# Optimization experiments

Hardware: AMD Instinct MI355X
Metric: run time of the kernel (lower is better)

The kernel has to match this reference:

```python
import jax, jax.numpy as jnp
import numpy as np

DIM = 256; CTX_DIM = 256; K = 7; SK = 5; NH = 4  # num_heads*2
HD = DIM // NH; SCALE = HD ** -0.5
H = 64; W = 64; HC = 56; WC = 56
LN_EPS = 1e-6; BN_EPS = 1e-5


def make_bias_idx(k, h, w):
    # Faithful port of ContMix.generate_idx + apply_rpb index construction.
    rs = 2 * k - 1
    idx_h = np.arange(k); idx_w = np.arange(k)
    idx_k = (idx_h[:, None] * rs + idx_w).reshape(-1)
    rep_h = np.ones(k, np.int64); rep_h[k // 2] = h - (k - 1)
    rep_w = np.ones(k, np.int64); rep_w[k // 2] = w - (k - 1)
    bias_hw = np.repeat(idx_h, rep_h)[:, None] * rs + np.repeat(idx_w, rep_w)  # (h, w)
    bias_idx = (bias_hw[..., None] + idx_k).reshape(-1, k * k)                 # (h*w, k^2)
    return jnp.asarray(bias_idx[::-1].copy())  # torch.flip along dim 0


def window_idx(n, k):
    # NATTEN-style clamped neighborhood window starts.
    s = np.clip(np.arange(n) - k // 2, 0, n - k)
    return jnp.asarray(s[:, None] + np.arange(k))  # (n, k)


BIDX1 = make_bias_idx(SK, H, W)
BIDX2 = make_bias_idx(K, H, W)
IDXI_S = window_idx(H, SK); IDXJ_S = window_idx(W, SK)
IDXI_L = window_idx(H, K);  IDXJ_L = window_idx(W, K)


def ln2d(x, g, b):
    # LayerNorm over channel dim per spatial location, x: (B, C, H, W)
    mu = x.mean(1, keepdims=True)
    var = ((x - mu) ** 2).mean(1, keepdims=True)
    return (x - mu) * jax.lax.rsqrt(var + LN_EPS) * g[None, :, None, None] + b[None, :, None, None]


def conv1x1(x, Wt):
    return jnp.einsum('oc,bchw->bohw', Wt, x)


def apply_rpb(attn, rpb, bias_idx, h, w):
    g = rpb.shape[0]
    r = rpb.reshape(g, -1)[:, bias_idx]  # (g, h*w, k^2)
    return attn + r.reshape(1, g, h, w, -1)


def na2d_av(attn, value, k, idx_i, idx_j):
    # attn: (B, G, H, W, k^2), value: (B, G, H, W, C)
    B, G, h, w, _ = attn.shape
    v = value[:, :, idx_i]        # (B, G, H, k, W, C)
    v = v[:, :, :, :, idx_j]      # (B, G, H, k, W, k, C)
    a = attn.reshape(B, G, h, w, k, k)
    return jnp.einsum('bghwpq,bghpwqc->bghwc', a, v)


def contmix_forward(x, ctx, Wq, gq, bq, Wk, gk, bk, Wproj, rpb1, rpb2, Wdy, bn_g, bn_b):
    B = x.shape[0]
    q = ln2d(conv1x1(x, Wq), gq, bq) * SCALE                       # (B, DIM, H, W)
    # AdaptiveAvgPool2d(7) on 56x56 -> exact 8x8 bins
    kctx = ctx.reshape(B, CTX_DIM, 7, HC // 7, 7, WC // 7).mean((3, 5))
    kf = ln2d(conv1x1(kctx, Wk), gk, bk)                            # (B, DIM, 7, 7)
    q = q.reshape(B, NH, HD, H * W)
    kf = kf.reshape(B, NH, HD, 49)
    wgt = jnp.einsum('bgcn,bgcl->bgnl', q, kf)                      # (B, 4, HW, 49)
    wgt = jnp.einsum('ml,bgnl->bgnm', Wproj, wgt)                   # (B, 4, HW, 74)
    wgt = wgt.reshape(B, NH, H, W, SK * SK + K * K)
    attn1 = wgt[:, :NH // 2, :, :, :SK * SK]                        # group1, 25
    attn2 = wgt[:, NH // 2:, :, :, SK * SK:]                        # group2, 49
    attn1 = jax.nn.softmax(apply_rpb(attn1, rpb1, BIDX1, H, W), -1)
    attn2 = jax.nn.softmax(apply_rpb(attn2, rpb2, BIDX2, H, W), -1)
    # 'b (m g c) h w -> m b g h w c', m=2, g=2
    v = x.reshape(B, 2, NH // 2, HD, H, W).transpose(1, 0, 2, 4, 5, 3)
    x1 = na2d_av(attn1, v[0], SK, IDXI_S, IDXJ_S)                   # (B, 2, H, W, HD)
    x2 = na2d_av(attn2, v[1], K, IDXI_L, IDXJ_L)
    out = jnp.concatenate([x1, x2], axis=1)                         # (B, 4, H, W, HD)
    out = out.transpose(0, 1, 4, 2, 3).reshape(B, DIM, H, W)
    out = conv1x1(out, Wdy)
    # BatchNorm2d in eval mode: running_mean=0, running_var=1
    out = out * (bn_g * jax.lax.rsqrt(jnp.float32(1.0) + BN_EPS))[None, :, None, None] + bn_b[None, :, None, None]
    return out


def setup_inputs() -> dict:
    key = jax.random.key(0)
    ks = jax.random.split(key, 10)
    d = {}
    d['x'] = jax.random.normal(ks[0], (4, DIM, H, W), jnp.float32)
    d['ctx'] = jax.random.normal(ks[1], (4, CTX_DIM, HC, WC), jnp.float32)
    d['Wq'] = jax.random.normal(ks[2], (DIM, DIM), jnp.float32) * 0.02
    d['gq'] = jnp.ones((DIM,), jnp.float32)
    d['bq'] = jnp.zeros((DIM,), jnp.float32)
    d['Wk'] = jax.random.normal(ks[3], (DIM, CTX_DIM), jnp.float32) * 0.02
    d['gk'] = jnp.ones((DIM,), jnp.float32)
    d['bk'] = jnp.zeros((DIM,), jnp.float32)
    d['Wproj'] = jax.random.normal(ks[4], (SK * SK + K * K, 49), jnp.float32) * 0.1
    d['rpb1'] = jax.random.normal(ks[5], (NH // 2, 2 * SK - 1, 2 * SK - 1), jnp.float32) * 0.02
    d['rpb2'] = jax.random.normal(ks[6], (NH // 2, 2 * K - 1, 2 * K - 1), jnp.float32) * 0.02
    d['Wdy'] = jax.random.normal(ks[7], (DIM, DIM), jnp.float32) * 0.02
    d['bn_g'] = jnp.ones((DIM,), jnp.float32)
    d['bn_b'] = jnp.zeros((DIM,), jnp.float32)
    return d


def reference(x, ctx, Wq, gq, bq, Wk, gk, bk, Wproj, rpb1, rpb2, Wdy, bn_g, bn_b):
    return contmix_forward(x, ctx, Wq, gq, bq, Wk, gk, bk, Wproj, rpb1, rpb2, Wdy, bn_g, bn_b)
```

## Files before the change

### kernel.cpp

```cpp
#include <hip/hip_runtime.h>

#define DEV __device__ __forceinline__

typedef __bf16 bf16x8 __attribute__((ext_vector_type(8)));
typedef __bf16 bf16x4 __attribute__((ext_vector_type(4)));
typedef float floatx4 __attribute__((ext_vector_type(4)));

__global__ __launch_bounds__(256)
void prep_kernel(const float* __restrict__ Wq, const float* __restrict__ Wdy,
                 const float* __restrict__ ctx, const float* __restrict__ x,
                 __bf16* __restrict__ wqb, __bf16* __restrict__ wdyb,
                 float* __restrict__ kctx, __bf16* __restrict__ xt) {
  __shared__ float tile[64][65];
  int bid = blockIdx.x, t = threadIdx.x;
  if (bid < 256) {
    int i = bid * 256 + t;
    wqb[i]  = (__bf16)Wq[i];
    wdyb[i] = (__bf16)Wdy[i];
  } else if (bid < 512) {
    int bc = (bid - 256) * 4 + (t >> 6);
    const float* src = ctx + (size_t)bc * (56 * 56);
    int w = t & 63;
#pragma unroll
    for (int pi = 0; pi < 7; ++pi) {
      float s = 0.f;
      if (w < 56) {
#pragma unroll
        for (int di = 0; di < 8; ++di) s += src[(pi * 8 + di) * 56 + w];
      }
      s += __shfl_down(s, 4);
      s += __shfl_down(s, 2);
      s += __shfl_down(s, 1);
      if (w < 56 && (w & 7) == 0)
        kctx[(size_t)bc * 49 + pi * 7 + (w >> 3)] = s * (1.f / 64.f);
    }
  } else {
    int idx = bid - 512;
    int b = idx >> 8, c0 = ((idx >> 6) & 3) * 64, n0 = (idx & 63) * 64;
    int lane = t & 63, rg = t >> 6;
    const float* src = x + ((size_t)b * 256 + c0) * 4096 + n0;
    for (int i = rg; i < 64; i += 4) tile[i][lane] = src[(size_t)i * 4096 + lane];
    __syncthreads();
    __bf16* dst = xt + ((size_t)b * 4096 + n0) * 256 + c0;
    for (int i = rg; i < 64; i += 4) dst[(size_t)i * 256 + lane] = (__bf16)tile[lane][i];
  }
}

__global__ __launch_bounds__(256)
void kf_ln_kernel(const float* __restrict__ kctx, const float* __restrict__ Wk,
                  const float* __restrict__ gk, const float* __restrict__ bk,
                  float* __restrict__ kf) {
  int b = blockIdx.x / 49, l = blockIdx.x % 49;
  __shared__ float xs[256];
  __shared__ float r1[4], r2[4];
  int o = threadIdx.x;
  xs[o] = kctx[((size_t)b * 256 + o) * 49 + l];
  __syncthreads();
  const float* wrow = Wk + (size_t)o * 256;
  float acc = 0.f;
#pragma unroll 8
  for (int c = 0; c < 256; c += 4) {
    float4 wv = *(const float4*)(wrow + c);
    acc += wv.x * xs[c] + wv.y * xs[c + 1] + wv.z * xs[c + 2] + wv.w * xs[c + 3];
  }
  float s1 = acc, s2 = acc * acc;
#pragma unroll
  for (int off = 32; off > 0; off >>= 1) {
    s1 += __shfl_down(s1, off);
    s2 += __shfl_down(s2, off);
  }
  int wv_ = o >> 6, ln = o & 63;
  if (ln == 0) { r1[wv_] = s1; r2[wv_] = s2; }
  __syncthreads();
  float mu  = (r1[0] + r1[1] + r1[2] + r1[3]) * (1.f / 256.f);
  float var = (r2[0] + r2[1] + r2[2] + r2[3]) * (1.f / 256.f) - mu * mu;
  float rstd = rsqrtf(var + 1e-6f);
  kf[((size_t)b * 256 + o) * 49 + l] = (acc - mu) * rstd * gk[o] + bk[o];
}

__global__ __launch_bounds__(256)
void kfp_kernel(const float* __restrict__ kf, const float* __restrict__ Wproj,
                __bf16* __restrict__ kfpT) {
  int bg = blockIdx.x; int b = bg >> 2, g = bg & 3;
  int m0 = blockIdx.y * 16;
  __shared__ float kfs[64][50];
  __shared__ float wps[16][50];
  int t = threadIdx.x;
  for (int i = t; i < 64 * 49; i += 256) {
    int d = i / 49, l = i % 49;
    kfs[d][l] = kf[((size_t)b * 256 + g * 64 + d) * 49 + l];
  }
  for (int i = t; i < 16 * 49; i += 256) {
    int m = i / 49, l = i % 49;
    wps[m][l] = (m0 + m < 74) ? Wproj[(m0 + m) * 49 + l] : 0.f;
  }
  __syncthreads();
  for (int i = t; i < 64 * 16; i += 256) {
    int d = i >> 4, m = i & 15;
    float s = 0.f;
    if (m0 + m < 74) {
#pragma unroll 7
      for (int l = 0; l < 49; ++l) s += kfs[d][l] * wps[m][l];
    }
    kfpT[(size_t)bg * 5120 + (m0 + m) * 64 + d] = (__bf16)s;
  }
}

DEV int rep_idx(int p, int kc, int t1, int sub) {
  return p < kc ? p : (p < t1 ? kc : p - sub);
}

template <int KK>
DEV void softmax_write(const float* wms, const float* rpb_s, __bf16* __restrict__ attnL,
                       int bg, int n_glob, int t) {
  constexpr int CNT = KK * KK;
  constexpr int RS  = 2 * KK - 1;
  constexpr int KC  = KK / 2;
  constexpr int T1  = KC + (64 - KK + 1);
  constexpr int SUB = 64 - KK;
  constexpr int MLO = (KK == 5) ? 0 : 25;
  constexpr int PW  = (KK == 5) ? 32 : 56;
  int h = n_glob >> 6, w = n_glob & 63;
  int rh = rep_idx(63 - h, KC, T1, SUB);
  int rw = rep_idx(63 - w, KC, T1, SUB);
  float vals[CNT];
  float mx = -1e30f;
#pragma unroll
  for (int m = 0; m < CNT; ++m) {
    int ki = m / KK, kj = m % KK;
    float v = wms[t * 81 + MLO + m] + rpb_s[(rh + ki) * RS + rw + kj];
    vals[m] = v; mx = fmaxf(mx, v);
  }
  float ssum = 0.f;
#pragma unroll
  for (int m = 0; m < CNT; ++m) { float e = __expf(vals[m] - mx); vals[m] = e; ssum += e; }
  float inv = 1.f / ssum;
  __bf16 hv[PW];
#pragma unroll
  for (int m = 0; m < PW; ++m) hv[m] = (__bf16)(m < CNT ? vals[m] * inv : 0.f);
  __bf16* ap = attnL + ((size_t)bg * 4096 + n_glob) * 56;
#pragma unroll
  for (int i = 0; i < PW / 8; ++i) *(bf16x8*)(ap + i * 8) = *(bf16x8*)&hv[i * 8];
}

__global__ __launch_bounds__(256, 1)
void qattn_kernel(const __bf16* __restrict__ Wb, const __bf16* __restrict__ XT,
                  const __bf16* __restrict__ kfpT,
                  const float* __restrict__ gq, const float* __restrict__ bq,
                  const float* __restrict__ rpb1, const float* __restrict__ rpb2,
                  __bf16* __restrict__ attnL) {
  __shared__ float wms[256 * 81];
  __shared__ float rpb_s[500];
  __shared__ float gqs[256], bqs[256];
  __shared__ float red_s[256], red_q[256];
  __shared__ float st_mu[64], st_rs[64];
  __bf16* As  = (__bf16*)wms;
  __bf16* Bs  = (__bf16*)wms + 8192;
  __bf16* Aat = (__bf16*)wms;

  int b  = blockIdx.z;
  int n0 = blockIdx.x * 64;
  int t  = threadIdx.x;
  int lane = t & 63, wv = t >> 6;
  int col = lane & 15, quad = lane >> 4;

  gqs[t] = gq[t] * 0.125f;
  bqs[t] = bq[t] * 0.125f;
  for (int i = t; i < 162; i += 256) rpb_s[i] = rpb1[i];
  for (int i = t; i < 338; i += 256) rpb_s[162 + i] = rpb2[i];

  floatx4 acc[4][4];
#pragma unroll
  for (int i = 0; i < 4; ++i)
#pragma unroll
    for (int j = 0; j < 4; ++j) acc[i][j] = {0.f, 0.f, 0.f, 0.f};

  int rowA = t >> 1, halfA = (t & 1) * 16;
  int rowB = t >> 2, kB = (t & 3) * 8;
  const __bf16* wp  = Wb + (size_t)rowA * 256 + halfA;
  const __bf16* wp2 = wp + 128 * 256;
  const __bf16* xp  = XT + ((size_t)b * 4096 + n0 + rowB) * 256 + kB;
  bf16x8 ra0a = *(const bf16x8*)wp;
  bf16x8 ra0b = *(const bf16x8*)(wp + 8);
  bf16x8 ra1a = *(const bf16x8*)wp2;
  bf16x8 ra1b = *(const bf16x8*)(wp2 + 8);
  bf16x8 rb   = *(const bf16x8*)xp;

  for (int c0 = 0; c0 < 256; c0 += 32) {
    *(bf16x8*)&As[rowA * 32 + halfA]             = ra0a;
    *(bf16x8*)&As[rowA * 32 + halfA + 8]         = ra0b;
    *(bf16x8*)&As[(128 + rowA) * 32 + halfA]     = ra1a;
    *(bf16x8*)&As[(128 + rowA) * 32 + halfA + 8] = ra1b;
    *(bf16x8*)&Bs[rowB * 32 + kB]                = rb;
    __syncthreads();
    if (c0 + 32 < 256) {
      ra0a = *(const bf16x8*)(wp  + c0 + 32);
      ra0b = *(const bf16x8*)(wp  + c0 + 40);
      ra1a = *(const bf16x8*)(wp2 + c0 + 32);
      ra1b = *(const bf16x8*)(wp2 + c0 + 40);
      rb   = *(const bf16x8*)(xp  + c0 + 32);
    }
    bf16x8 fa[4], fb[4];
#pragma unroll
    for (int i = 0; i < 4; ++i)
      fa[i] = *(const bf16x8*)&As[(wv * 64 + i * 16 + col) * 32 + quad * 8];
#pragma unroll
    for (int j = 0; j < 4; ++j)
      fb[j] = *(const bf16x8*)&Bs[(j * 16 + col) * 32 + quad * 8];
#pragma unroll
    for (int i = 0; i < 4; ++i)
#pragma unroll
      for (int j = 0; j < 4; ++j)
        acc[i][j] = __builtin_amdgcn_mfma_f32_16x16x32_bf16(fa[i], fb[j], acc[i][j], 0, 0, 0);
    __syncthreads();
  }

  float sj[4], qj[4];
#pragma unroll
  for (int j = 0; j < 4; ++j) {
    float s = 0.f, q = 0.f;
#pragma unroll
    for (int i = 0; i < 4; ++i)
#pragma unroll
      for (int r = 0; r < 4; ++r) { float v = acc[i][j][r]; s += v; q += v * v; }
    s += __shfl_xor(s, 16); s += __shfl_xor(s, 32);
    q += __shfl_xor(q, 16); q += __shfl_xor(q, 32);
    sj[j] = s; qj[j] = q;
  }
  if (quad == 0) {
#pragma unroll
    for (int j = 0; j < 4; ++j) {
      red_s[wv * 64 + j * 16 + col] = sj[j];
      red_q[wv * 64 + j * 16 + col] = qj[j];
    }
  }
  __syncthreads();
  if (t < 64) {
    float s = red_s[t] + red_s[64 + t] + red_s[128 + t] + red_s[192 + t];
    float q = red_q[t] + red_q[64 + t] + red_q[128 + t] + red_q[192 + t];
    float mu  = s * (1.f / 256.f);
    float var = q * (1.f / 256.f) - mu * mu;
    st_mu[t] = mu;
    st_rs[t] = rsqrtf(var + 1e-6f);
  }
  __syncthreads();

#pragma unroll
  for (int j = 0; j < 4; ++j) {
    float mu = st_mu[j * 16 + col], rs = st_rs[j * 16 + col];
#pragma unroll
    for (int i = 0; i < 4; ++i) {
      __bf16 pk[4];
#pragma unroll
      for (int r = 0; r < 4; ++r) {
        int o = wv * 64 + i * 16 + quad * 4 + r;
        pk[r] = (__bf16)((acc[i][j][r] - mu) * rs * gqs[o] + bqs[o]);
      }
      *(bf16x4*)&Aat[(wv * 64 + j * 16 + col) * 72 + i * 16 + quad * 4] = *(bf16x4*)pk;
    }
  }
  __syncthreads();

  bf16x8 fa2[2][4], fb2[2][5];
  const __bf16* kp = kfpT + (size_t)(b * 4 + wv) * 5120;
#pragma unroll
  for (int ks = 0; ks < 2; ++ks) {
#pragma unroll
    for (int a = 0; a < 4; ++a)
      fa2[ks][a] = *(const bf16x8*)&Aat[(wv * 64 + a * 16 + col) * 72 + ks * 32 + quad * 8];
#pragma unroll
    for (int nt = 0; nt < 5; ++nt)
      fb2[ks][nt] = *(const bf16x8*)&kp[(nt * 16 + col) * 64 + ks * 32 + quad * 8];
  }
  floatx4 acc2[4][5];
#pragma unroll
  for (int a = 0; a < 4; ++a)
#pragma unroll
    for (int nt = 0; nt < 5; ++nt) acc2[a][nt] = {0.f, 0.f, 0.f, 0.f};
#pragma unroll
  for (int ks = 0; ks < 2; ++ks)
#pragma unroll
    for (int a = 0; a < 4; ++a)
#pragma unroll
      for (int nt = 0; nt < 5; ++nt)
        acc2[a][nt] = __builtin_amdgcn_mfma_f32_16x16x32_bf16(fa2[ks][a], fb2[ks][nt], acc2[a][nt], 0, 0, 0);
  __syncthreads();

#pragma unroll
  for (int a = 0; a < 4; ++a)
#pragma unroll
    for (int nt = 0; nt < 5; ++nt)
#pragma unroll
      for (int r = 0; r < 4; ++r)
        wms[(wv * 64 + a * 16 + quad * 4 + r) * 81 + nt * 16 + col] = acc2[a][nt][r];
  __syncthreads();

  int g2 = t >> 6;
  int n_glob = n0 + (t & 63);
  int bg = b * 4 + g2;
  if (g2 < 2) softmax_write<5>(wms, rpb_s + g2 * 81,              attnL, bg, n_glob, t);
  else        softmax_write<7>(wms, rpb_s + 162 + (g2 - 2) * 169, attnL, bg, n_glob, t);
}

template <int MODE>
__global__ __launch_bounds__(256, 2)
void conv_mfma_kernel(const __bf16* __restrict__ Wb, const __bf16* __restrict__ Xin,
                      void* __restrict__ Yout, float* __restrict__ stats,
                      const float* __restrict__ bn_g, const float* __restrict__ bn_b) {
  int b  = blockIdx.z;
  int n0 = blockIdx.x * 128;
  int o0 = blockIdx.y * 128;
  __shared__ __bf16 As[128 * 32];
  __shared__ __bf16 Bs[128 * 32];
  int t = threadIdx.x;
  int lane = t & 63, wv = t >> 6;
  int mq = (wv & 1) * 64, nq = (wv >> 1) * 64;
  int col = lane & 15, quad = lane >> 4;
  floatx4 acc[4][4];
#pragma unroll
  for (int i = 0; i < 4; ++i)
#pragma unroll
    for (int j = 0; j < 4; ++j) acc[i][j] = {0.f, 0.f, 0.f, 0.f};
  int sm = t >> 1, sk = (t & 1) << 4;
  for (int c0 = 0; c0 < 256; c0 += 32) {
    const __bf16* wsrc = Wb + (size_t)(o0 + sm) * 256 + c0 + sk;
    *(bf16x8*)&As[sm * 32 + sk]     = *(const bf16x8*)wsrc;
    *(bf16x8*)&As[sm * 32 + sk + 8] = *(const bf16x8*)(wsrc + 8);
    const __bf16* xsrc;
    if (MODE == 0) {
      xsrc = Xin + ((size_t)b * 4096 + n0 + sm) * 256 + c0 + sk;
    } else {
      int c = c0 + sk, g = c >> 6, c64 = c & 63;
      xsrc = Xin + (((size_t)(b * 4 + g)) * 4096 + n0 + sm) * 64 + c64;
    }
    *(bf16x8*)&Bs[sm * 32 + sk]     = *(const bf16x8*)xsrc;
    *(bf16x8*)&Bs[sm * 32 + sk + 8] = *(const bf16x8*)(xsrc + 8);
    __syncthreads();
    bf16x8 fa[4], fb[4];
#pragma unroll
    for (int i = 0; i < 4; ++i)
      fa[i] = *(const bf16x8*)&As[(mq + i * 16 + col) * 32 + quad * 8];
#pragma unroll
    for (int j = 0; j < 4; ++j)
      fb[j] = *(const bf16x8*)&Bs[(nq + j * 16 + col) * 32 + quad * 8];
#pragma unroll
    for (int i = 0; i < 4; ++i)
#pragma unroll
      for (int j = 0; j < 4; ++j)
        acc[i][j] = __builtin_amdgcn_mfma_f32_16x16x32_bf16(fa[i], fb[j], acc[i][j], 0, 0, 0);
    __syncthreads();
  }
  {
    float* Yf = (float*)Yout + (size_t)b * 256 * 4096;
#pragma unroll
    for (int i = 0; i < 4; ++i) {
#pragma unroll
      for (int r = 0; r < 4; ++r) {
        int o = o0 + mq + i * 16 + quad * 4 + r;
        float scale = bn_g[o] * 0.9999950000374997f;
        float shift = bn_b[o];
        float* yrow = Yf + (size_t)o * 4096 + n0 + nq + col;
#pragma unroll
        for (int j = 0; j < 4; ++j) yrow[j * 16] = acc[i][j][r] * scale + shift;
      }
    }
  }
}

template <int KK>
DEV void na2d_body(const __bf16* __restrict__ attnL, const __bf16* __restrict__ XT,
                   __bf16* __restrict__ midT, __bf16* xs, int bg, int h0, int chalf, int t) {
  constexpr int CNT = KK * KK, KC = KK / 2, SMAX = 64 - KK;
  constexpr int ROWS = KK + 3;
  constexpr int PW = (KK == 5) ? 32 : 56;
  int b = bg >> 2, g = bg & 3;
  int si0 = min(max(h0 - KC, 0), SMAX);
  {
    int sn = t >> 2, sc = t & 3;
    const __bf16* src = XT + ((size_t)b * 4096 + sn) * 256 + g * 64 + chalf * 32 + sc * 8;
#pragma unroll
    for (int r = 0; r < ROWS; ++r) {
      int gr = min(si0 + r, 63);
      *(bf16x8*)&xs[(r * 64 + sn) * 40 + sc * 8] = *(const bf16x8*)(src + (size_t)gr * 64 * 256);
    }
  }
  __syncthreads();
  int w = t >> 2, cg = t & 3;
  int sj = min(max(w - KC, 0), SMAX);
#pragma unroll
  for (int h4 = 0; h4 < 4; ++h4) {
    int h = h0 + h4;
    int base = min(max(h - KC, 0), SMAX) - si0;
    bf16x8 avh[PW / 8];
    const __bf16* ap = attnL + ((size_t)bg * 4096 + h * 64 + w) * 56;
#pragma unroll
    for (int i = 0; i < PW / 8; ++i) avh[i] = *(const bf16x8*)(ap + i * 8);
    float av[CNT];
#pragma unroll
    for (int m = 0; m < CNT; ++m) av[m] = (float)avh[m / 8][m % 8];
    float acc[8] = {};
#pragma unroll
    for (int p = 0; p < KK; ++p) {
      const __bf16* xr = &xs[((base + p) * 64 + sj) * 40 + cg * 8];
#pragma unroll
      for (int q = 0; q < KK; ++q) {
        bf16x8 v = *(const bf16x8*)(xr + q * 40);
        float a = av[p * KK + q];
#pragma unroll
        for (int e = 0; e < 8; ++e) acc[e] += a * (float)v[e];
      }
    }
    __bf16 hv[8];
#pragma unroll
    for (int e = 0; e < 8; ++e) hv[e] = (__bf16)acc[e];
    *(bf16x8*)&midT[((size_t)bg * 4096 + h * 64 + w) * 64 + chalf * 32 + cg * 8] = *(bf16x8*)hv;
  }
}

__global__ __launch_bounds__(256)
void na2d_kernel(const __bf16* __restrict__ attnL, const __bf16* __restrict__ XT,
                 __bf16* __restrict__ midT) {
  __shared__ __bf16 xs[10 * 64 * 40];
  int bg = blockIdx.x, h0 = blockIdx.y * 4, chalf = blockIdx.z, t = threadIdx.x;
  if ((bg & 3) < 2) na2d_body<5>(attnL, XT, midT, xs, bg, h0, chalf, t);
  else              na2d_body<7>(attnL, XT, midT, xs, bg, h0, chalf, t);
}

extern "C" void kernel_launch(void* const* d_in, const int* in_sizes, int n_in,
                              void* d_out, int out_size, void* d_ws, size_t ws_size,
                              hipStream_t stream) {
  const float* x     = (const float*)d_in[0];
  const float* ctx   = (const float*)d_in[1];
  const float* Wq    = (const float*)d_in[2];
  const float* gq    = (const float*)d_in[3];
  const float* bq    = (const float*)d_in[4];
  const float* Wk    = (const float*)d_in[5];
  const float* gk    = (const float*)d_in[6];
  const float* bk    = (const float*)d_in[7];
  const float* Wproj = (const float*)d_in[8];
  const float* rpb1  = (const float*)d_in[9];
  const float* rpb2  = (const float*)d_in[10];
  const float* Wdy   = (const float*)d_in[11];
  const float* bn_g  = (const float*)d_in[12];
  const float* bn_b  = (const float*)d_in[13];
  float* out = (float*)d_out;

  float* ws     = (float*)d_ws;
  float* kctx   = ws;
  float* kf     = kctx + 50176;
  __bf16* attnL = (__bf16*)(kf + 50176);
  __bf16* wqb   = attnL + 3670016;
  __bf16* wdyb  = wqb + 65536;
  __bf16* kfpT  = wdyb + 65536;
  __bf16* XT    = kfpT + 81920;
  __bf16* midT  = XT + 4194304;

  prep_kernel<<<dim3(1536), dim3(256), 0, stream>>>(Wq, Wdy, ctx, x, wqb, wdyb, kctx, XT);
  kf_ln_kernel<<<dim3(196), dim3(256), 0, stream>>>(kctx, Wk, gk, bk, kf);
  kfp_kernel<<<dim3(16, 5), dim3(256), 0, stream>>>(kf, Wproj, kfpT);
  qattn_kernel<<<dim3(64, 1, 4), dim3(256), 0, stream>>>(wqb, XT, kfpT, gq, bq, rpb1, rpb2, attnL);
  na2d_kernel<<<dim3(16, 16, 2), dim3(256), 0, stream>>>(attnL, XT, midT);
  conv_mfma_kernel<1><<<dim3(32, 2, 4), dim3(256), 0, stream>>>(wdyb, midT, out, nullptr, bn_g, bn_b);
}
```

Before: 162.1 us.

## Halve qattn spatial tile for more blocks and add register prefetch to conv GEMM

The fused q-projection/attention kernel now handles 32 spatial positions per block instead of 64. That halves its shared-memory footprint and accumulator count, allows two blocks per CU, and doubles the grid to 512 blocks so the 256 CUs are better filled. The trade-off is that every block reloads the full weight matrix, and only half the threads do the softmax phase. Separately, the final conv GEMM now prefetches the next K-slice into registers before the shared-memory stores, overlapping global loads with MFMA work.

Measured after the change: 163.9 us. Within noise of the previous version (+1.1%).

```diff
diff --git a/kernel.cpp b/kernel.cpp
--- a/kernel.cpp
+++ b/kernel.cpp
@@ -112,7 +112,7 @@
 
 template <int KK>
 DEV void softmax_write(const float* wms, const float* rpb_s, __bf16* __restrict__ attnL,
-                       int bg, int n_glob, int t) {
+                       int bg, int n_glob, int row) {
   constexpr int CNT = KK * KK;
   constexpr int RS  = 2 * KK - 1;
   constexpr int KC  = KK / 2;
@@ -128,7 +128,7 @@
 #pragma unroll
   for (int m = 0; m < CNT; ++m) {
     int ki = m / KK, kj = m % KK;
-    float v = wms[t * 81 + MLO + m] + rpb_s[(rh + ki) * RS + rw + kj];
+    float v = wms[row * 81 + MLO + m] + rpb_s[(rh + ki) * RS + rw + kj];
     vals[m] = v; mx = fmaxf(mx, v);
   }
   float ssum = 0.f;
@@ -143,23 +143,23 @@
   for (int i = 0; i < PW / 8; ++i) *(bf16x8*)(ap + i * 8) = *(bf16x8*)&hv[i * 8];
 }
 
-__global__ __launch_bounds__(256, 1)
+__global__ __launch_bounds__(256, 2)
 void qattn_kernel(const __bf16* __restrict__ Wb, const __bf16* __restrict__ XT,
                   const __bf16* __restrict__ kfpT,
                   const float* __restrict__ gq, const float* __restrict__ bq,
                   const float* __restrict__ rpb1, const float* __restrict__ rpb2,
                   __bf16* __restrict__ attnL) {
-  __shared__ float wms[256 * 81];
+  __shared__ float wms[128 * 81];
   __shared__ float rpb_s[500];
   __shared__ float gqs[256], bqs[256];
-  __shared__ float red_s[256], red_q[256];
-  __shared__ float st_mu[64], st_rs[64];
+  __shared__ float red_s[128], red_q[128];
+  __shared__ float st_mu[32], st_rs[32];
   __bf16* As  = (__bf16*)wms;
   __bf16* Bs  = (__bf16*)wms + 8192;
   __bf16* Aat = (__bf16*)wms;
 
   int b  = blockIdx.z;
-  int n0 = blockIdx.x * 64;
+  int n0 = blockIdx.x * 32;
   int t  = threadIdx.x;
   int lane = t & 63, wv = t >> 6;
   int col = lane & 15, quad = lane >> 4;
@@ -169,55 +169,52 @@
   for (int i = t; i < 162; i += 256) rpb_s[i] = rpb1[i];
   for (int i = t; i < 338; i += 256) rpb_s[162 + i] = rpb2[i];
 
-  floatx4 acc[4][4];
+  floatx4 acc[4][2];
 #pragma unroll
   for (int i = 0; i < 4; ++i)
 #pragma unroll
-    for (int j = 0; j < 4; ++j) acc[i][j] = {0.f, 0.f, 0.f, 0.f};
-
-  int rowA = t >> 1, halfA = (t & 1) * 16;
-  int rowB = t >> 2, kB = (t & 3) * 8;
-  const __bf16* wp  = Wb + (size_t)rowA * 256 + halfA;
-  const __bf16* wp2 = wp + 128 * 256;
-  const __bf16* xp  = XT + ((size_t)b * 4096 + n0 + rowB) * 256 + kB;
-  bf16x8 ra0a = *(const bf16x8*)wp;
-  bf16x8 ra0b = *(const bf16x8*)(wp + 8);
-  bf16x8 ra1a = *(const bf16x8*)wp2;
-  bf16x8 ra1b = *(const bf16x8*)(wp2 + 8);
-  bf16x8 rb   = *(const bf16x8*)xp;
+    for (int j = 0; j < 2; ++j) acc[i][j] = {0.f, 0.f, 0.f, 0.f};
+
+  const __bf16* wp = Wb + (size_t)t * 256;
+  int rowB = t >> 3, kB = (t & 7) * 4;
+  const __bf16* xp = XT + ((size_t)b * 4096 + n0 + rowB) * 256 + kB;
+  bf16x8 ra0 = *(const bf16x8*)(wp + 0);
+  bf16x8 ra1 = *(const bf16x8*)(wp + 8);
+  bf16x8 ra2 = *(const bf16x8*)(wp + 16);
+  bf16x8 ra3 = *(const bf16x8*)(wp + 24);
+  bf16x4 rb  = *(const bf16x4*)xp;
 
   for (int c0 = 0; c0 < 256; c0 += 32) {
-    *(bf16x8*)&As[rowA * 32 + halfA]             = ra0a;
-    *(bf16x8*)&As[rowA * 32 + halfA + 8]         = ra0b;
-    *(bf16x8*)&As[(128 + rowA) * 32 + halfA]     = ra1a;
-    *(bf16x8*)&As[(128 + rowA) * 32 + halfA + 8] = ra1b;
-    *(bf16x8*)&Bs[rowB * 32 + kB]                = rb;
+    *(bf16x8*)&As[t * 32 + 0]  = ra0;
+    *(bf16x8*)&As[t * 32 + 8]  = ra1;
+    *(bf16x8*)&As[t * 32 + 16] = ra2;
+    *(bf16x8*)&As[t * 32 + 24] = ra3;
+    *(bf16x4*)&Bs[rowB * 32 + kB] = rb;
     __syncthreads();
     if (c0 + 32 < 256) {
-      ra0a = *(const bf16x8*)(wp  + c0 + 32);
-      ra0b = *(const bf16x8*)(wp  + c0 + 40);
-      ra1a = *(const bf16x8*)(wp2 + c0 + 32);
-      ra1b = *(const bf16x8*)(wp2 + c0 + 40);
-      rb   = *(const bf16x8*)(xp  + c0 + 32);
-    }
-    bf16x8 fa[4], fb[4];
+      ra0 = *(const bf16x8*)(wp + c0 + 32);
+      ra1 = *(const bf16x8*)(wp + c0 + 40);
+      ra2 = *(const bf16x8*)(wp + c0 + 48);
+      ra3 = *(const bf16x8*)(wp + c0 + 56);
+      rb  = *(const bf16x4*)(xp + c0 + 32);
+    }
+    bf16x8 fa[4], fb[2];
 #pragma unroll
     for (int i = 0; i < 4; ++i)
       fa[i] = *(const bf16x8*)&As[(wv * 64 + i * 16 + col) * 32 + quad * 8];
 #pragma unroll
-    for (int j = 0; j < 4; ++j)
+    for (int j = 0; j < 2; ++j)
       fb[j] = *(const bf16x8*)&Bs[(j * 16 + col) * 32 + quad * 8];
 #pragma unroll
     for (int i = 0; i < 4; ++i)
 #pragma unroll
-      for (int j = 0; j < 4; ++j)
+      for (int j = 0; j < 2; ++j)
         acc[i][j] = __builtin_amdgcn_mfma_f32_16x16x32_bf16(fa[i], fb[j], acc[i][j], 0, 0, 0);
     __syncthreads();
   }
 
-  float sj[4], qj[4];
-#pragma unroll
-  for (int j = 0; j < 4; ++j) {
+#pragma unroll
+  for (int j = 0; j < 2; ++j) {
     float s = 0.f, q = 0.f;
 #pragma unroll
     for (int i = 0; i < 4; ++i)
@@ -225,19 +222,15 @@
       for (int r = 0; r < 4; ++r) { float v = acc[i][j][r]; s += v; q += v * v; }
     s += __shfl_xor(s, 16); s += __shfl_xor(s, 32);
     q += __shfl_xor(q, 16); q += __shfl_xor(q, 32);
-    sj[j] = s; qj[j] = q;
-  }
-  if (quad == 0) {
-#pragma unroll
-    for (int j = 0; j < 4; ++j) {
-      red_s[wv * 64 + j * 16 + col] = sj[j];
-      red_q[wv * 64 + j * 16 + col] = qj[j];
-    }
-  }
-  __syncthreads();
-  if (t < 64) {
-    float s = red_s[t] + red_s[64 + t] + red_s[128 + t] + red_s[192 + t];
-    float q = red_q[t] + red_q[64 + t] + red_q[128 + t] + red_q[192 + t];
+    if (quad == 0) {
+      red_s[wv * 32 + j * 16 + col] = s;
+      red_q[wv * 32 + j * 16 + col] = q;
+    }
+  }
+  __syncthreads();
+  if (t < 32) {
+    float s = red_s[t] + red_s[32 + t] + red_s[64 + t] + red_s[96 + t];
+    float q = red_q[t] + red_q[32 + t] + red_q[64 + t] + red_q[96 + t];
     float mu  = s * (1.f / 256.f);
     float var = q * (1.f / 256.f) - mu * mu;
     st_mu[t] = mu;
@@ -246,7 +239,7 @@
   __syncthreads();
 
 #pragma unroll
-  for (int j = 0; j < 4; ++j) {
+  for (int j = 0; j < 2; ++j) {
     float mu = st_mu[j * 16 + col], rs = st_rs[j * 16 + col];
 #pragma unroll
     for (int i = 0; i < 4; ++i) {
@@ -256,50 +249,52 @@
         int o = wv * 64 + i * 16 + quad * 4 + r;
         pk[r] = (__bf16)((acc[i][j][r] - mu) * rs * gqs[o] + bqs[o]);
       }
-      *(bf16x4*)&Aat[(wv * 64 + j * 16 + col) * 72 + i * 16 + quad * 4] = *(bf16x4*)pk;
-    }
-  }
-  __syncthreads();
-
-  bf16x8 fa2[2][4], fb2[2][5];
+      *(bf16x4*)&Aat[(wv * 32 + j * 16 + col) * 72 + i * 16 + quad * 4] = *(bf16x4*)pk;
+    }
+  }
+  __syncthreads();
+
+  bf16x8 fa2[2][2], fb2[2][5];
   const __bf16* kp = kfpT + (size_t)(b * 4 + wv) * 5120;
 #pragma unroll
   for (int ks = 0; ks < 2; ++ks) {
 #pragma unroll
-    for (int a = 0; a < 4; ++a)
-      fa2[ks][a] = *(const bf16x8*)&Aat[(wv * 64 + a * 16 + col) * 72 + ks * 32 + quad * 8];
+    for (int a = 0; a < 2; ++a)
+      fa2[ks][a] = *(const bf16x8*)&Aat[(wv * 32 + a * 16 + col) * 72 + ks * 32 + quad * 8];
 #pragma unroll
     for (int nt = 0; nt < 5; ++nt)
       fb2[ks][nt] = *(const bf16x8*)&kp[(nt * 16 + col) * 64 + ks * 32 + quad * 8];
   }
-  floatx4 acc2[4][5];
-#pragma unroll
-  for (int a = 0; a < 4; ++a)
+  floatx4 acc2[2][5];
+#pragma unroll
+  for (int a = 0; a < 2; ++a)
 #pragma unroll
     for (int nt = 0; nt < 5; ++nt) acc2[a][nt] = {0.f, 0.f, 0.f, 0.f};
 #pragma unroll
   for (int ks = 0; ks < 2; ++ks)
 #pragma unroll
-    for (int a = 0; a < 4; ++a)
+    for (int a = 0; a < 2; ++a)
 #pragma unroll
       for (int nt = 0; nt < 5; ++nt)
         acc2[a][nt] = __builtin_amdgcn_mfma_f32_16x16x32_bf16(fa2[ks][a], fb2[ks][nt], acc2[a][nt], 0, 0, 0);
   __syncthreads();
 
 #pragma unroll
-  for (int a = 0; a < 4; ++a)
+  for (int a = 0; a < 2; ++a)
 #pragma unroll
     for (int nt = 0; nt < 5; ++nt)
 #pragma unroll
       for (int r = 0; r < 4; ++r)
-        wms[(wv * 64 + a * 16 + quad * 4 + r) * 81 + nt * 16 + col] = acc2[a][nt][r];
-  __syncthreads();
-
-  int g2 = t >> 6;
-  int n_glob = n0 + (t & 63);
-  int bg = b * 4 + g2;
-  if (g2 < 2) softmax_write<5>(wms, rpb_s + g2 * 81,              attnL, bg, n_glob, t);
-  else        softmax_write<7>(wms, rpb_s + 162 + (g2 - 2) * 169, attnL, bg, n_glob, t);
+        wms[(wv * 32 + a * 16 + quad * 4 + r) * 81 + nt * 16 + col] = acc2[a][nt][r];
+  __syncthreads();
+
+  if (t < 128) {
+    int g2 = t >> 5;
+    int n_glob = n0 + (t & 31);
+    int bg = b * 4 + g2;
+    if (g2 < 2) softmax_write<5>(wms, rpb_s + g2 * 81,              attnL, bg, n_glob, t);
+    else        softmax_write<7>(wms, rpb_s + 162 + (g2 - 2) * 169, attnL, bg, n_glob, t);
+  }
 }
 
 template <int MODE>
@@ -322,20 +317,33 @@
 #pragma unroll
     for (int j = 0; j < 4; ++j) acc[i][j] = {0.f, 0.f, 0.f, 0.f};
   int sm = t >> 1, sk = (t & 1) << 4;
-  for (int c0 = 0; c0 < 256; c0 += 32) {
-    const __bf16* wsrc = Wb + (size_t)(o0 + sm) * 256 + c0 + sk;
-    *(bf16x8*)&As[sm * 32 + sk]     = *(const bf16x8*)wsrc;
-    *(bf16x8*)&As[sm * 32 + sk + 8] = *(const bf16x8*)(wsrc + 8);
-    const __bf16* xsrc;
+  const __bf16* wp = Wb + (size_t)(o0 + sm) * 256 + sk;
+  auto xaddr = [&](int c0) -> const __bf16* {
     if (MODE == 0) {
-      xsrc = Xin + ((size_t)b * 4096 + n0 + sm) * 256 + c0 + sk;
+      return Xin + ((size_t)b * 4096 + n0 + sm) * 256 + c0 + sk;
     } else {
       int c = c0 + sk, g = c >> 6, c64 = c & 63;
-      xsrc = Xin + (((size_t)(b * 4 + g)) * 4096 + n0 + sm) * 64 + c64;
-    }
-    *(bf16x8*)&Bs[sm * 32 + sk]     = *(const bf16x8*)xsrc;
-    *(bf16x8*)&Bs[sm * 32 + sk + 8] = *(const bf16x8*)(xsrc + 8);
+      return Xin + (((size_t)(b * 4 + g)) * 4096 + n0 + sm) * 64 + c64;
+    }
+  };
+  bf16x8 wa0 = *(const bf16x8*)wp;
+  bf16x8 wa1 = *(const bf16x8*)(wp + 8);
+  const __bf16* x0 = xaddr(0);
+  bf16x8 xb0 = *(const bf16x8*)x0;
+  bf16x8 xb1 = *(const bf16x8*)(x0 + 8);
+  for (int c0 = 0; c0 < 256; c0 += 32) {
+    *(bf16x8*)&As[sm * 32 + sk]     = wa0;
+    *(bf16x8*)&As[sm * 32 + sk + 8] = wa1;
+    *(bf16x8*)&Bs[sm * 32 + sk]     = xb0;
+    *(bf16x8*)&Bs[sm * 32 + sk + 8] = xb1;
     __syncthreads();
+    if (c0 + 32 < 256) {
+      wa0 = *(const bf16x8*)(wp + c0 + 32);
+      wa1 = *(const bf16x8*)(wp + c0 + 40);
+      const __bf16* xn = xaddr(c0 + 32);
+      xb0 = *(const bf16x8*)xn;
+      xb1 = *(const bf16x8*)(xn + 8);
+    }
     bf16x8 fa[4], fb[4];
 #pragma unroll
     for (int i = 0; i < 4; ++i)
@@ -458,7 +466,7 @@
   prep_kernel<<<dim3(1536), dim3(256), 0, stream>>>(Wq, Wdy, ctx, x, wqb, wdyb, kctx, XT);
   kf_ln_kernel<<<dim3(196), dim3(256), 0, stream>>>(kctx, Wk, gk, bk, kf);
   kfp_kernel<<<dim3(16, 5), dim3(256), 0, stream>>>(kf, Wproj, kfpT);
-  qattn_kernel<<<dim3(64, 1, 4), dim3(256), 0, stream>>>(wqb, XT, kfpT, gq, bq, rpb1, rpb2, attnL);
+  qattn_kernel<<<dim3(128, 1, 4), dim3(256), 0, stream>>>(wqb, XT, kfpT, gq, bq, rpb1, rpb2, attnL);
   na2d_kernel<<<dim3(16, 16, 2), dim3(256), 0, stream>>>(attnL, XT, midT);
   conv_mfma_kernel<1><<<dim3(32, 2, 4), dim3(256), 0, stream>>>(wdyb, midT, out, nullptr, bn_g, bn_b);
 }
```
